# Optimization experiments

Measured on AMD Instinct MI355X. Metric: run time of the kernel, lower is better.

The kernel has to match this reference:

```python
import jax, jax.numpy as jnp
import numpy as np

R, C, M, G, H, W, NUM_POS = 2048, 81, 28, 100, 512, 512, 512


def roi_align_1s(feats, bidx, boxes, Mo):
    """RoI align with 1 sample per bin (bin center), spatial_scale=1.0, aligned=False.
    feats: [G,H,W]; bidx: [R] int (which feat map per roi); boxes: [R,4] (x1,y1,x2,y2).
    Returns [R,Mo,Mo]."""
    Hh, Ww = feats.shape[-2], feats.shape[-1]
    x1, y1, x2, y2 = boxes[:, 0], boxes[:, 1], boxes[:, 2], boxes[:, 3]
    grid = (jnp.arange(Mo, dtype=boxes.dtype) + 0.5) / Mo  # bin centers in [0,1)
    gx = x1[:, None] + grid[None, :] * (x2 - x1)[:, None]  # [R,Mo]
    gy = y1[:, None] + grid[None, :] * (y2 - y1)[:, None]  # [R,Mo]
    x = gx[:, None, :]  # [R,1,Mo]
    y = gy[:, :, None]  # [R,Mo,1]
    valid = (x > -1.0) & (x < Ww) & (y > -1.0) & (y < Hh)  # [R,Mo,Mo]
    xc = jnp.clip(x, 0.0, Ww - 1.0)
    yc = jnp.clip(y, 0.0, Hh - 1.0)
    x0 = jnp.floor(xc).astype(jnp.int32)
    y0 = jnp.floor(yc).astype(jnp.int32)
    x1i = jnp.minimum(x0 + 1, Ww - 1)
    y1i = jnp.minimum(y0 + 1, Hh - 1)
    lx = xc - x0
    ly = yc - y0
    b = bidx[:, None, None]
    v00 = feats[b, y0, x0]
    v01 = feats[b, y0, x1i]
    v10 = feats[b, y1i, x0]
    v11 = feats[b, y1i, x1i]
    val = (v00 * (1.0 - ly) * (1.0 - lx) + v01 * (1.0 - ly) * lx
           + v10 * ly * (1.0 - lx) + v11 * ly * lx)
    return jnp.where(valid, val, 0.0)


def setup_inputs() -> dict:
    key = jax.random.key(0)
    ks = jax.random.split(key, 8)
    class_logit = jax.random.normal(ks[0], (R, C), jnp.float32)
    box_regression = jax.random.normal(ks[1], (R, 4 * C), jnp.float32)
    regression_target = jax.random.normal(ks[2], (NUM_POS, 4), jnp.float32)
    mask_logit = jax.random.normal(ks[3], (R, C, M, M), jnp.float32)
    u = jax.random.uniform(ks[4], (R, 4), jnp.float32)
    bx1 = u[:, 0] * (W - 96.0)
    by1 = u[:, 1] * (H - 96.0)
    proposal = jnp.stack([bx1, by1, bx1 + 16.0 + u[:, 2] * 64.0, by1 + 16.0 + u[:, 3] * 64.0], axis=1)
    matched_idx = jax.random.randint(ks[5], (R,), 0, G)
    label = jax.random.randint(ks[6], (R,), 0, C)
    gt_mask = (jax.random.uniform(ks[7], (G, H, W)) > 0.5).astype(jnp.float32)
    return dict(class_logit=class_logit, box_regression=box_regression,
                regression_target=regression_target, mask_logit=mask_logit,
                proposal=proposal, gt_mask=gt_mask, matched_idx=matched_idx,
                label=label, num_pos=NUM_POS)


def reference(class_logit, box_regression, regression_target, mask_logit,
              proposal, gt_mask, matched_idx, label, num_pos):
    N = class_logit.shape[0]
    num_gt = gt_mask.shape[0]
    # ---- fastrcnn_loss ----
    logp = jax.nn.log_softmax(class_logit, axis=-1)
    cls_loss = -jnp.take_along_axis(logp, label[:, None], axis=1).mean()
    breg = box_regression.reshape(N, -1, 4)[:num_pos]          # [P, C, 4]
    pred = breg[jnp.arange(num_pos), label[:num_pos]]          # [P, 4]
    d = jnp.abs(pred - regression_target)
    box_loss = jnp.where(d < 1.0, 0.5 * d * d, d - 0.5).sum() / N  # smooth_l1(sum)/N
    # ---- maskrcnn_loss_average_per_gt ----
    Mo = mask_logit.shape[-1]
    mask_target = roi_align_1s(gt_mask, matched_idx, proposal, Mo)   # [N,M,M]
    sel = mask_logit[jnp.arange(N), label]                            # [N,M,M]
    # stable BCE-with-logits, reduction='none'
    bce = jnp.maximum(sel, 0.0) - sel * mask_target + jnp.log1p(jnp.exp(-jnp.abs(sel)))
    per_roi = bce.mean(axis=(-2, -1))                                 # [N]
    seg_sum = jax.ops.segment_sum(per_roi, matched_idx, num_segments=num_gt)
    cnt = jax.ops.segment_sum(jnp.ones_like(per_roi), matched_idx, num_segments=num_gt)
    per_gt = jnp.where(cnt > 0, seg_sum / jnp.maximum(cnt, 1.0), 0.0)  # [G]
    return jnp.concatenate([cls_loss[None], box_loss[None], per_gt])   # [2+G]
```

## Files before the change

### kernel.cpp

```cpp
#include <hip/hip_runtime.h>
#include <hip/hip_bf16.h>

#define RR 2048
#define CC 81
#define MM 28
#define GG 100
#define HH 512
#define WW 512

__global__ void init_kernel(float* out, float* ws) {
    int t = threadIdx.x;
    for (int i = t; i < 102; i += blockDim.x) out[i] = 0.0f;
    for (int i = t; i < 2 * GG; i += blockDim.x) ws[i] = 0.0f;
}

__global__ __launch_bounds__(256) void fused_kernel(
    const float* __restrict__ class_logit,
    const float* __restrict__ box_reg,
    const float* __restrict__ reg_tgt,
    const float* __restrict__ mask_logit,
    const float* __restrict__ proposal,
    const float* __restrict__ gt_mask,
    const int* __restrict__ matched_idx,
    const int* __restrict__ label,
    const int* __restrict__ num_pos_p,
    float* __restrict__ out,
    float* __restrict__ seg_sum,
    float* __restrict__ cnt) {
    int lane = threadIdx.x & 63;
    int r = blockIdx.x * 4 + (threadIdx.x >> 6);

    int lbl = label[r];
    int m_idx = matched_idx[r];

    int num_pos = *num_pos_p;
    if (r < num_pos) {
        float bl = 0.0f;
        if (lane < 4) {
            float pred = box_reg[(size_t)r * (4 * CC) + lbl * 4 + lane];
            float d = fabsf(pred - reg_tgt[r * 4 + lane]);
            bl = (d < 1.0f) ? 0.5f * d * d : d - 0.5f;
        }
        bl += __shfl_down(bl, 2);
        bl += __shfl_down(bl, 1);
        if (lane == 0) atomicAdd(out + 1, bl * (1.0f / (float)RR));
    }

    {
        const float* rowp = class_logit + (size_t)r * CC;
        float v0 = (lane < CC) ? rowp[lane] : -1e30f;
        float v1 = (lane + 64 < CC) ? rowp[lane + 64] : -1e30f;
        float m = fmaxf(v0, v1);
        #pragma unroll
        for (int off = 32; off > 0; off >>= 1) m = fmaxf(m, __shfl_down(m, off));
        m = __shfl(m, 0);
        float s = 0.0f;
        if (lane < CC) s += __expf(v0 - m);
        if (lane + 64 < CC) s += __expf(v1 - m);
        #pragma unroll
        for (int off = 32; off > 0; off >>= 1) s += __shfl_down(s, off);
        if (lane == 0) {
            float lse = m + __logf(s);
            atomicAdd(out + 0, (lse - rowp[lbl]) * (1.0f / (float)RR));
        }
    }

    {
        float x1 = proposal[r * 4 + 0];
        float y1 = proposal[r * 4 + 1];
        float x2 = proposal[r * 4 + 2];
        float y2 = proposal[r * 4 + 3];
        float bw = x2 - x1, bh = y2 - y1;

        const float4* sel4 = (const float4*)(mask_logit + ((size_t)r * CC + lbl) * (MM * MM));
        const float* fm = gt_mask + (size_t)m_idx * (HH * WW);

        float acc = 0.0f;
        for (int i4 = lane; i4 < (MM * MM) / 4; i4 += 64) {
            float4 sv = sel4[i4];
            float svv[4] = {sv.x, sv.y, sv.z, sv.w};
            int pbase = i4 * 4;
            #pragma unroll
            for (int j = 0; j < 4; j++) {
                int p = pbase + j;
                int py = p / MM, px = p - py * MM;
                float gx = x1 + ((px + 0.5f) / (float)MM) * bw;
                float gy = y1 + ((py + 0.5f) / (float)MM) * bh;
                bool valid = (gx > -1.0f) && (gx < (float)WW) && (gy > -1.0f) && (gy < (float)HH);
                float xc = fminf(fmaxf(gx, 0.0f), (float)(WW - 1));
                float yc = fminf(fmaxf(gy, 0.0f), (float)(HH - 1));
                int x0 = (int)floorf(xc);
                int y0 = (int)floorf(yc);
                int x1i = min(x0 + 1, WW - 1);
                int y1i = min(y0 + 1, HH - 1);
                float lx = xc - (float)x0;
                float ly = yc - (float)y0;
                float v00 = fm[y0 * WW + x0];
                float v01 = fm[y0 * WW + x1i];
                float v10 = fm[y1i * WW + x0];
                float v11 = fm[y1i * WW + x1i];
                float val = v00 * (1.0f - ly) * (1.0f - lx) + v01 * (1.0f - ly) * lx +
                            v10 * ly * (1.0f - lx) + v11 * ly * lx;
                float tgt = valid ? val : 0.0f;
                float s = svv[j];
                acc += fmaxf(s, 0.0f) - s * tgt + log1pf(__expf(-fabsf(s)));
            }
        }
        #pragma unroll
        for (int off = 32; off > 0; off >>= 1) acc += __shfl_down(acc, off);
        if (lane == 0) {
            atomicAdd(seg_sum + m_idx, acc * (1.0f / (float)(MM * MM)));
            atomicAdd(cnt + m_idx, 1.0f);
        }
    }
}

__global__ void fin_kernel(const float* __restrict__ seg_sum,
                           const float* __restrict__ cnt,
                           float* __restrict__ out) {
    int g = threadIdx.x + blockIdx.x * blockDim.x;
    if (g < GG) {
        float c = cnt[g];
        out[2 + g] = (c > 0.0f) ? seg_sum[g] / fmaxf(c, 1.0f) : 0.0f;
    }
}

extern "C" void kernel_launch(void* const* d_in, const int* in_sizes, int n_in,
                              void* d_out, int out_size, void* d_ws, size_t ws_size,
                              hipStream_t stream) {
    const float* class_logit    = (const float*)d_in[0];
    const float* box_regression = (const float*)d_in[1];
    const float* regression_tgt = (const float*)d_in[2];
    const float* mask_logit     = (const float*)d_in[3];
    const float* proposal       = (const float*)d_in[4];
    const float* gt_mask        = (const float*)d_in[5];
    const int*   matched_idx    = (const int*)d_in[6];
    const int*   label          = (const int*)d_in[7];
    const int*   num_pos        = (const int*)d_in[8];

    float* out = (float*)d_out;
    float* seg_sum = (float*)d_ws;
    float* cnt = seg_sum + GG;

    init_kernel<<<1, 256, 0, stream>>>(out, seg_sum);

    fused_kernel<<<RR / 4, 256, 0, stream>>>(
        class_logit, box_regression, regression_tgt, mask_logit, proposal,
        gt_mask, matched_idx, label, num_pos, out, seg_sum, cnt);

    fin_kernel<<<1, 128, 0, stream>>>(seg_sum, cnt, out);
}
```

Before: 645.6 us.

## Use one block per RoI and replace global atomics with two-stage reduction

Each RoI now gets a full 256-thread block, so the 196 float4 mask pixels are spread across threads instead of looped over one wave. The class and box losses run on separate waves in parallel. Per-RoI partials go to workspace, and a single finishing kernel reduces them with shared-memory atomics, which removes the init kernel and the global atomics. This adds a block-level sync, a serial single-block final pass over 2048 entries, and idle threads (60 of 256) in the mask phase.

```diff
diff --git a/kernel.cpp b/kernel.cpp
--- a/kernel.cpp
+++ b/kernel.cpp
@@ -1,5 +1,4 @@
 #include <hip/hip_runtime.h>
-#include <hip/hip_bf16.h>
 
 #define RR 2048
 #define CC 81
@@ -7,12 +6,6 @@
 #define GG 100
 #define HH 512
 #define WW 512
-
-__global__ void init_kernel(float* out, float* ws) {
-    int t = threadIdx.x;
-    for (int i = t; i < 102; i += blockDim.x) out[i] = 0.0f;
-    for (int i = t; i < 2 * GG; i += blockDim.x) ws[i] = 0.0f;
-}
 
 __global__ __launch_bounds__(256) void fused_kernel(
     const float* __restrict__ class_logit,
@@ -24,29 +17,19 @@
     const int* __restrict__ matched_idx,
     const int* __restrict__ label,
     const int* __restrict__ num_pos_p,
-    float* __restrict__ out,
-    float* __restrict__ seg_sum,
-    float* __restrict__ cnt) {
-    int lane = threadIdx.x & 63;
-    int r = blockIdx.x * 4 + (threadIdx.x >> 6);
+    float* __restrict__ per_roi,
+    float* __restrict__ cls_part,
+    float* __restrict__ box_part) {
+    const int r = blockIdx.x;
+    const int t = threadIdx.x;
+    const int wave = t >> 6;
+    const int lane = t & 63;
+    const int lbl = label[r];
+    const int m_idx = matched_idx[r];
 
-    int lbl = label[r];
-    int m_idx = matched_idx[r];
+    __shared__ float red[4];
 
-    int num_pos = *num_pos_p;
-    if (r < num_pos) {
-        float bl = 0.0f;
-        if (lane < 4) {
-            float pred = box_reg[(size_t)r * (4 * CC) + lbl * 4 + lane];
-            float d = fabsf(pred - reg_tgt[r * 4 + lane]);
-            bl = (d < 1.0f) ? 0.5f * d * d : d - 0.5f;
-        }
-        bl += __shfl_down(bl, 2);
-        bl += __shfl_down(bl, 1);
-        if (lane == 0) atomicAdd(out + 1, bl * (1.0f / (float)RR));
-    }
-
-    {
+    if (wave == 0) {
         const float* rowp = class_logit + (size_t)r * CC;
         float v0 = (lane < CC) ? rowp[lane] : -1e30f;
         float v1 = (lane + 64 < CC) ? rowp[lane + 64] : -1e30f;
@@ -59,69 +42,111 @@
         if (lane + 64 < CC) s += __expf(v1 - m);
         #pragma unroll
         for (int off = 32; off > 0; off >>= 1) s += __shfl_down(s, off);
-        if (lane == 0) {
-            float lse = m + __logf(s);
-            atomicAdd(out + 0, (lse - rowp[lbl]) * (1.0f / (float)RR));
+        if (lane == 0) cls_part[r] = (m + __logf(s)) - rowp[lbl];
+    } else if (wave == 1) {
+        int np = *num_pos_p;
+        if (r < np) {
+            float bl = 0.0f;
+            if (lane < 4) {
+                float pred = box_reg[(size_t)r * (4 * CC) + lbl * 4 + lane];
+                float d = fabsf(pred - reg_tgt[r * 4 + lane]);
+                bl = (d < 1.0f) ? 0.5f * d * d : d - 0.5f;
+            }
+            bl += __shfl_down(bl, 2);
+            bl += __shfl_down(bl, 1);
+            if (lane == 0) box_part[r] = bl;
         }
     }
 
-    {
-        float x1 = proposal[r * 4 + 0];
-        float y1 = proposal[r * 4 + 1];
-        float x2 = proposal[r * 4 + 2];
-        float y2 = proposal[r * 4 + 3];
-        float bw = x2 - x1, bh = y2 - y1;
+    float x1 = proposal[r * 4 + 0];
+    float y1 = proposal[r * 4 + 1];
+    float bw = proposal[r * 4 + 2] - x1;
+    float bh = proposal[r * 4 + 3] - y1;
+    const float inv = 1.0f / (float)MM;
 
+    float acc = 0.0f;
+    if (t < (MM * MM) / 4) {
         const float4* sel4 = (const float4*)(mask_logit + ((size_t)r * CC + lbl) * (MM * MM));
         const float* fm = gt_mask + (size_t)m_idx * (HH * WW);
-
-        float acc = 0.0f;
-        for (int i4 = lane; i4 < (MM * MM) / 4; i4 += 64) {
-            float4 sv = sel4[i4];
-            float svv[4] = {sv.x, sv.y, sv.z, sv.w};
-            int pbase = i4 * 4;
-            #pragma unroll
-            for (int j = 0; j < 4; j++) {
-                int p = pbase + j;
-                int py = p / MM, px = p - py * MM;
-                float gx = x1 + ((px + 0.5f) / (float)MM) * bw;
-                float gy = y1 + ((py + 0.5f) / (float)MM) * bh;
-                bool valid = (gx > -1.0f) && (gx < (float)WW) && (gy > -1.0f) && (gy < (float)HH);
-                float xc = fminf(fmaxf(gx, 0.0f), (float)(WW - 1));
-                float yc = fminf(fmaxf(gy, 0.0f), (float)(HH - 1));
-                int x0 = (int)floorf(xc);
-                int y0 = (int)floorf(yc);
-                int x1i = min(x0 + 1, WW - 1);
-                int y1i = min(y0 + 1, HH - 1);
-                float lx = xc - (float)x0;
-                float ly = yc - (float)y0;
-                float v00 = fm[y0 * WW + x0];
-                float v01 = fm[y0 * WW + x1i];
-                float v10 = fm[y1i * WW + x0];
-                float v11 = fm[y1i * WW + x1i];
-                float val = v00 * (1.0f - ly) * (1.0f - lx) + v01 * (1.0f - ly) * lx +
-                            v10 * ly * (1.0f - lx) + v11 * ly * lx;
-                float tgt = valid ? val : 0.0f;
-                float s = svv[j];
-                acc += fmaxf(s, 0.0f) - s * tgt + log1pf(__expf(-fabsf(s)));
-            }
-        }
+        float4 sv = sel4[t];
+        float svv[4] = {sv.x, sv.y, sv.z, sv.w};
+        int pbase = t * 4;
         #pragma unroll
-        for (int off = 32; off > 0; off >>= 1) acc += __shfl_down(acc, off);
-        if (lane == 0) {
-            atomicAdd(seg_sum + m_idx, acc * (1.0f / (float)(MM * MM)));
-            atomicAdd(cnt + m_idx, 1.0f);
+        for (int j = 0; j < 4; j++) {
+            int p = pbase + j;
+            int py = p / MM;
+            int px = p - py * MM;
+            float gx = x1 + (((float)px + 0.5f) * inv) * bw;
+            float gy = y1 + (((float)py + 0.5f) * inv) * bh;
+            bool valid = (gx > -1.0f) && (gx < (float)WW) && (gy > -1.0f) && (gy < (float)HH);
+            float xc = fminf(fmaxf(gx, 0.0f), (float)(WW - 1));
+            float yc = fminf(fmaxf(gy, 0.0f), (float)(HH - 1));
+            int x0 = (int)xc;
+            int y0 = (int)yc;
+            int x1i = min(x0 + 1, WW - 1);
+            int y1i = min(y0 + 1, HH - 1);
+            float lx = xc - (float)x0;
+            float ly = yc - (float)y0;
+            const float* row0 = fm + y0 * WW;
+            const float* row1 = fm + y1i * WW;
+            float v00 = row0[x0], v01 = row0[x1i];
+            float v10 = row1[x0], v11 = row1[x1i];
+            float a = v00 + lx * (v01 - v00);
+            float b = v10 + lx * (v11 - v10);
+            float val = a + ly * (b - a);
+            float tgt = valid ? val : 0.0f;
+            float s = svv[j];
+            acc += fmaxf(s, 0.0f) - s * tgt + __logf(1.0f + __expf(-fabsf(s)));
         }
     }
+    #pragma unroll
+    for (int off = 32; off > 0; off >>= 1) acc += __shfl_down(acc, off);
+    if (lane == 0) red[wave] = acc;
+    __syncthreads();
+    if (t == 0)
+        per_roi[r] = (red[0] + red[1] + red[2] + red[3]) * (1.0f / (float)(MM * MM));
 }
 
-__global__ void fin_kernel(const float* __restrict__ seg_sum,
-                           const float* __restrict__ cnt,
-                           float* __restrict__ out) {
-    int g = threadIdx.x + blockIdx.x * blockDim.x;
-    if (g < GG) {
-        float c = cnt[g];
-        out[2 + g] = (c > 0.0f) ? seg_sum[g] / fmaxf(c, 1.0f) : 0.0f;
+__global__ __launch_bounds__(256) void fin_kernel(
+    const float* __restrict__ per_roi,
+    const float* __restrict__ cls_part,
+    const float* __restrict__ box_part,
+    const int* __restrict__ matched_idx,
+    const int* __restrict__ num_pos_p,
+    float* __restrict__ out) {
+    __shared__ float segs[GG];
+    __shared__ float cnts[GG];
+    __shared__ float red[8];
+    int t = threadIdx.x;
+    for (int i = t; i < GG; i += 256) { segs[i] = 0.0f; cnts[i] = 0.0f; }
+    __syncthreads();
+
+    float cacc = 0.0f, bacc = 0.0f;
+    for (int r = t; r < RR; r += 256) {
+        cacc += cls_part[r];
+        int g = matched_idx[r];
+        atomicAdd(&segs[g], per_roi[r]);
+        atomicAdd(&cnts[g], 1.0f);
+    }
+    int np = *num_pos_p;
+    for (int r = t; r < np; r += 256) bacc += box_part[r];
+
+    #pragma unroll
+    for (int off = 32; off > 0; off >>= 1) {
+        cacc += __shfl_down(cacc, off);
+        bacc += __shfl_down(bacc, off);
+    }
+    int wave = t >> 6, lane = t & 63;
+    if (lane == 0) { red[wave] = cacc; red[4 + wave] = bacc; }
+    __syncthreads();
+
+    if (t == 0) {
+        out[0] = (red[0] + red[1] + red[2] + red[3]) * (1.0f / (float)RR);
+        out[1] = (red[4] + red[5] + red[6] + red[7]) * (1.0f / (float)RR);
+    }
+    if (t < GG) {
+        float c = cnts[t];
+        out[2 + t] = (c > 0.0f) ? segs[t] / fmaxf(c, 1.0f) : 0.0f;
     }
 }
 
@@ -139,14 +164,14 @@
     const int*   num_pos        = (const int*)d_in[8];
 
     float* out = (float*)d_out;
-    float* seg_sum = (float*)d_ws;
-    float* cnt = seg_sum + GG;
+    float* per_roi  = (float*)d_ws;
+    float* cls_part = per_roi + RR;
+    float* box_part = cls_part + RR;
 
-    init_kernel<<<1, 256, 0, stream>>>(out, seg_sum);
+    fused_kernel<<<RR, 256, 0, stream>>>(
+        class_logit, box_regression, regression_tgt, mask_logit, proposal,
+        gt_mask, matched_idx, label, num_pos, per_roi, cls_part, box_part);
 
-    fused_kernel<<<RR / 4, 256, 0, stream>>>(
-        class_logit, box_regression, regression_tgt, mask_logit, proposal,
-        gt_mask, matched_idx, label, num_pos, out, seg_sum, cnt);
-
-    fin_kernel<<<1, 128, 0, stream>>>(seg_sum, cnt, out);
+    fin_kernel<<<1, 256, 0, stream>>>(per_roi, cls_part, box_part,
+                                      matched_idx, num_pos, out);
 }
```

Measured after the change: 619.2 us. -4.1%, faster.
